# Optimization experiments

Measured on AMD Instinct MI355X. Metric: run time of the kernel, lower is better.

Reference implementation:

```python
import jax, jax.numpy as jnp
import numpy as np

# E2M1 (FP4) value table: low 3 bits magnitude, bit 3 sign (indices 8..15 negative)
FP4_TABLE = jnp.array([0.0, 0.5, 1.0, 1.5, 2.0, 3.0, 4.0, 6.0,
                       0.0, -0.5, -1.0, -1.5, -2.0, -3.0, -4.0, -6.0], dtype=jnp.float32)
FP4_BLOCK = 32  # per-row 1x32 scale groups


def dequant_fp4(packed, scale):
    """packed: [E, O, I//2] uint8 (two e2m1 nibbles per byte, low nibble first),
    scale: [E, O, I//32] float32 (e8m0, i.e. powers of two). Returns [E, O, I] float32."""
    lo = (packed & 15).astype(jnp.int32)
    hi = ((packed >> 4) & 15).astype(jnp.int32)
    # interleave low, high nibbles along the input dim (matches torch stack(...,-1).flatten)
    vals = FP4_TABLE[jnp.stack([lo, hi], axis=-1)]  # [E, O, I//2, 2]
    w = vals.reshape(packed.shape[0], packed.shape[1], packed.shape[2] * 2)
    return w * jnp.repeat(scale, FP4_BLOCK, axis=-1)


def setup_inputs() -> dict:
    T, H, F, E, K = 2048, 2048, 1024, 16, 4
    key = jax.random.key(0)
    k = jax.random.split(key, 8)
    hidden_states = jax.random.normal(k[0], (T, H), dtype=jnp.float32)
    topk_weights = jax.nn.softmax(jax.random.normal(k[1], (T, K)), axis=-1)
    topk_ids = jax.random.randint(k[2], (T, K), 0, E, dtype=jnp.int32)
    # checkpoint-native packed FP4 expert weights + e8m0 (power-of-two) scales
    gate_up_weight = jax.random.randint(k[3], (E, 2 * F, H // 2), 0, 256, dtype=jnp.int32).astype(jnp.uint8)
    gate_up_scale = jnp.exp2(jax.random.randint(k[4], (E, 2 * F, H // 32), -8, -5).astype(jnp.float32))
    down_weight = jax.random.randint(k[5], (E, H, F // 2), 0, 256, dtype=jnp.int32).astype(jnp.uint8)
    down_scale = jnp.exp2(jax.random.randint(k[6], (E, H, F // 32), -8, -5).astype(jnp.float32))
    return {"hidden_states": hidden_states, "topk_weights": topk_weights, "topk_ids": topk_ids,
            "gate_up_weight": gate_up_weight, "gate_up_scale": gate_up_scale,
            "down_weight": down_weight, "down_scale": down_scale}


def reference(hidden_states, topk_weights, topk_ids, gate_up_weight, gate_up_scale, down_weight, down_scale):
    # 1. dequantize checkpoint-native FP4 experts to dense float weights
    w_gate_up = dequant_fp4(gate_up_weight, gate_up_scale)  # [E, 2F, H]
    w_down = dequant_fp4(down_weight, down_scale)           # [E, H, F]
    T = hidden_states.shape[0]
    E = w_gate_up.shape[0]
    # 2. scatter routing weights into a dense [T, E] combine matrix
    combine = jnp.zeros((T, E), dtype=hidden_states.dtype)
    combine = combine.at[jnp.arange(T)[:, None], topk_ids].add(topk_weights)
    # 3. grouped expert GEMM (exact dense dispatch over experts)
    gu = jnp.einsum('th,eoh->teo', hidden_states, w_gate_up)  # [T, E, 2F]
    gate, up = jnp.split(gu, 2, axis=-1)                       # gate = first ffn_dim rows
    act = jax.nn.silu(gate) * up                               # SwiGLU (swiglu_limit=0 -> no clamping)
    act = act * combine[:, :, None]                            # fold routing weights into activations
    return jnp.einsum('tef,ehf->th', act, w_down)              # [T, H]
```

## Files before the change

kernel.cpp:

```cpp
#include <hip/hip_runtime.h>
#include <stdint.h>

#define T_TOK 2048
#define HD 2048
#define FD 1024
#define NE 16
#define NPAIR 8192
#define BM 128
#define MAXTILES 80
#define LDK 40

typedef short bf16x8 __attribute__((ext_vector_type(8)));
typedef float f32x4 __attribute__((ext_vector_type(4)));
typedef unsigned short u16;

static __device__ __forceinline__ u16 f2bf(float f) {
  uint32_t u = __float_as_uint(f);
  u += 0x7FFFu + ((u >> 16) & 1u);
  return (u16)(u >> 16);
}

static __device__ __forceinline__ float fp4_val(uint32_t nib, float scale) {
  uint32_t mag = nib & 7u;
  uint32_t big = ((126u + (mag >> 1)) << 23) | ((mag & 1u) << 22);
  uint32_t small = (0u - (mag & 1u)) & 0x3F000000u;
  uint32_t bits = (mag >= 2u) ? big : small;
  bits |= (nib & 8u) << 28;
  return __uint_as_float(bits) * scale;
}

static __device__ __forceinline__ uint32_t dq_byte(uint32_t b, float scale) {
  float lo = fp4_val(b & 15u, scale);
  float hi = fp4_val((b >> 4) & 15u, scale);
  return ((uint32_t)(__float_as_uint(lo) >> 16)) | (__float_as_uint(hi) & 0xFFFF0000u);
}

__global__ void cast_kernel(const float* __restrict__ x, u16* __restrict__ xb) {
  int i = blockIdx.x * 256 + threadIdx.x;
  float4 v = ((const float4*)x)[i];
  ushort4 o;
  o.x = f2bf(v.x); o.y = f2bf(v.y); o.z = f2bf(v.z); o.w = f2bf(v.w);
  ((ushort4*)xb)[i] = o;
}

__global__ void zero_kernel(float4* __restrict__ out) {
  out[blockIdx.x * 256 + threadIdx.x] = float4{0.f, 0.f, 0.f, 0.f};
}

__global__ void route_kernel(const int* __restrict__ ids, const float* __restrict__ tw,
                             int* __restrict__ rows, float* __restrict__ rw,
                             int* __restrict__ te) {
  __shared__ int cnt[NE], base[NE], run[NE];
  int tid = threadIdx.x;
  if (tid < NE) { cnt[tid] = 0; run[tid] = 0; }
  __syncthreads();
  for (int i = tid; i < NPAIR; i += 256) atomicAdd(&cnt[ids[i]], 1);
  __syncthreads();
  if (tid == 0) {
    int cum = 0;
    for (int e = 0; e < NE; ++e) {
      base[e] = cum;
      int nt = (cnt[e] + BM - 1) >> 7;
      for (int j = 0; j < nt; ++j) te[(cum >> 7) + j] = e;
      cum += nt << 7;
    }
    for (int t = cum >> 7; t < MAXTILES; ++t) te[t] = -1;
  }
  __syncthreads();
  for (int i = tid; i < MAXTILES * BM; i += 256) { rows[i] = -1; rw[i] = 0.f; }
  __syncthreads();
  for (int i = tid; i < NPAIR; i += 256) {
    int e = ids[i];
    int p = base[e] + atomicAdd(&run[e], 1);
    rows[p] = i >> 2;
    rw[p] = tw[i];
  }
}

__global__ __launch_bounds__(256) void gemm1_kernel(
    const u16* __restrict__ xb, const int* __restrict__ gup32,
    const float* __restrict__ gus, const int* __restrict__ rows,
    const float* __restrict__ rw, const int* __restrict__ te,
    u16* __restrict__ act) {
  const int tile = blockIdx.y;
  const int e = te[tile];
  if (e < 0) return;
  const int f0 = blockIdx.x * 64;

  __shared__ u16 sA[BM * LDK];
  __shared__ u16 sBg[64 * LDK];
  __shared__ u16 sBu[64 * LDK];
  __shared__ int rows_s[BM];
  __shared__ float rw_s[BM];

  const int tid = threadIdx.x;
  if (tid < BM) {
    rows_s[tid] = rows[tile * BM + tid];
    rw_s[tid] = rw[tile * BM + tid];
  }
  __syncthreads();

  const int sm = tid >> 1;
  const int skh = tid & 1;
  int arow = rows_s[sm];
  arow = arow < 0 ? 0 : arow;
  const u16* aptr = xb + (size_t)arow * HD + skh * 16;
  u16* sAp = &sA[sm * LDK + skh * 16];

  const int bn = (tid & 127) >> 1;
  const int isUp = tid >> 7;
  const int o = isUp * 1024 + f0 + bn;
  const int* bptr = gup32 + (size_t)(e * 2048 + o) * (HD / 2) + skh * 8;
  const float* sptr = gus + (size_t)(e * 2048 + o) * (HD / 32);
  u16* sBp = (isUp ? sBu : sBg) + bn * LDK + skh * 16;

  const int lane = tid & 63;
  const int wid = tid >> 6;
  const int wm = wid >> 1, wn = wid & 1;
  const int q = lane >> 4, c = lane & 15;

  f32x4 Cg[4][2], Cu[4][2];
#pragma unroll
  for (int s = 0; s < 4; ++s)
#pragma unroll
    for (int t2 = 0; t2 < 2; ++t2) {
      Cg[s][t2] = f32x4{0.f, 0.f, 0.f, 0.f};
      Cu[s][t2] = f32x4{0.f, 0.f, 0.f, 0.f};
    }

  for (int kk = 0; kk < HD; kk += 32) {
    uint4 av0 = *(const uint4*)(aptr + kk);
    uint4 av1 = *(const uint4*)(aptr + kk + 8);
    int4 w0 = *(const int4*)(bptr + (kk >> 1));
    int4 w1 = *(const int4*)(bptr + (kk >> 1) + 4);
    float sc = sptr[kk >> 5];
    uint32_t d[8];
    d[0] = dq_byte((uint32_t)w0.x, sc);
    d[1] = dq_byte((uint32_t)w0.y, sc);
    d[2] = dq_byte((uint32_t)w0.z, sc);
    d[3] = dq_byte((uint32_t)w0.w, sc);
    d[4] = dq_byte((uint32_t)w1.x, sc);
    d[5] = dq_byte((uint32_t)w1.y, sc);
    d[6] = dq_byte((uint32_t)w1.z, sc);
    d[7] = dq_byte((uint32_t)w1.w, sc);
    *(uint4*)sAp = av0;
    *(uint4*)(sAp + 8) = av1;
    *(uint4*)sBp = make_uint4(d[0], d[1], d[2], d[3]);
    *(uint4*)(sBp + 8) = make_uint4(d[4], d[5], d[6], d[7]);
    __syncthreads();

    bf16x8 af[4], bgf[2], buf_[2];
#pragma unroll
    for (int s = 0; s < 4; ++s)
      af[s] = *(const bf16x8*)&sA[(wm * 64 + s * 16 + c) * LDK + q * 8];
#pragma unroll
    for (int t2 = 0; t2 < 2; ++t2) {
      bgf[t2] = *(const bf16x8*)&sBg[(wn * 32 + t2 * 16 + c) * LDK + q * 8];
      buf_[t2] = *(const bf16x8*)&sBu[(wn * 32 + t2 * 16 + c) * LDK + q * 8];
    }
#pragma unroll
    for (int s = 0; s < 4; ++s)
#pragma unroll
      for (int t2 = 0; t2 < 2; ++t2) {
        Cg[s][t2] = __builtin_amdgcn_mfma_f32_16x16x32_bf16(af[s], bgf[t2], Cg[s][t2], 0, 0, 0);
        Cu[s][t2] = __builtin_amdgcn_mfma_f32_16x16x32_bf16(af[s], buf_[t2], Cu[s][t2], 0, 0, 0);
      }
    __syncthreads();
  }

#pragma unroll
  for (int s = 0; s < 4; ++s) {
    const int mlb = wm * 64 + s * 16 + q * 4;
#pragma unroll
    for (int t2 = 0; t2 < 2; ++t2) {
      const int fg = f0 + wn * 32 + t2 * 16 + c;
#pragma unroll
      for (int r = 0; r < 4; ++r) {
        const int ml = mlb + r;
        float g = Cg[s][t2][r];
        float u = Cu[s][t2][r];
        float aval = g / (1.f + __expf(-g)) * u * rw_s[ml];
        act[(size_t)(tile * BM + ml) * FD + fg] = f2bf(aval);
      }
    }
  }
}

__global__ __launch_bounds__(256) void gemm2_kernel(
    const u16* __restrict__ act, const int* __restrict__ dwn32,
    const float* __restrict__ dsc, const int* __restrict__ rows,
    const int* __restrict__ te, float* __restrict__ out) {
  const int tile = blockIdx.y;
  const int e = te[tile];
  if (e < 0) return;
  const int h0 = blockIdx.x * 64;

  __shared__ u16 sA[BM * LDK];
  __shared__ u16 sB[64 * LDK];
  __shared__ int rows_s[BM];

  const int tid = threadIdx.x;
  if (tid < BM) rows_s[tid] = rows[tile * BM + tid];
  __syncthreads();

  const int sm = tid >> 1;
  const int skh = tid & 1;
  const u16* aptr = act + (size_t)(tile * BM + sm) * FD + skh * 16;
  u16* sAp = &sA[sm * LDK + skh * 16];

  const int bn2 = tid >> 2;
  const int kq = tid & 3;
  const int* bptr = dwn32 + (size_t)(e * 2048 + h0 + bn2) * (FD / 2) + kq * 4;
  const float* sptr = dsc + (size_t)(e * 2048 + h0 + bn2) * (FD / 32);
  u16* sBp = &sB[bn2 * LDK + kq * 8];

  const int lane = tid & 63;
  const int wid = tid >> 6;
  const int wm = wid >> 1, wn = wid & 1;
  const int q = lane >> 4, c = lane & 15;

  f32x4 Cd[4][2];
#pragma unroll
  for (int s = 0; s < 4; ++s)
#pragma unroll
    for (int t2 = 0; t2 < 2; ++t2) Cd[s][t2] = f32x4{0.f, 0.f, 0.f, 0.f};

  for (int kk = 0; kk < FD; kk += 32) {
    uint4 av0 = *(const uint4*)(aptr + kk);
    uint4 av1 = *(const uint4*)(aptr + kk + 8);
    int4 w = *(const int4*)(bptr + (kk >> 1));
    float sc = sptr[kk >> 5];
    uint32_t d[4];
    d[0] = dq_byte((uint32_t)w.x, sc);
    d[1] = dq_byte((uint32_t)w.y, sc);
    d[2] = dq_byte((uint32_t)w.z, sc);
    d[3] = dq_byte((uint32_t)w.w, sc);
    *(uint4*)sAp = av0;
    *(uint4*)(sAp + 8) = av1;
    *(uint4*)sBp = make_uint4(d[0], d[1], d[2], d[3]);
    __syncthreads();

    bf16x8 af[4], bf_[2];
#pragma unroll
    for (int s = 0; s < 4; ++s)
      af[s] = *(const bf16x8*)&sA[(wm * 64 + s * 16 + c) * LDK + q * 8];
#pragma unroll
    for (int t2 = 0; t2 < 2; ++t2)
      bf_[t2] = *(const bf16x8*)&sB[(wn * 32 + t2 * 16 + c) * LDK + q * 8];
#pragma unroll
    for (int s = 0; s < 4; ++s)
#pragma unroll
      for (int t2 = 0; t2 < 2; ++t2)
        Cd[s][t2] = __builtin_amdgcn_mfma_f32_16x16x32_bf16(af[s], bf_[t2], Cd[s][t2], 0, 0, 0);
    __syncthreads();
  }

#pragma unroll
  for (int s = 0; s < 4; ++s) {
    const int mlb = wm * 64 + s * 16 + q * 4;
#pragma unroll
    for (int t2 = 0; t2 < 2; ++t2) {
      const int hg = h0 + wn * 32 + t2 * 16 + c;
#pragma unroll
      for (int r = 0; r < 4; ++r) {
        int token = rows_s[mlb + r];
        if (token >= 0) atomicAdd(&out[(size_t)token * HD + hg], Cd[s][t2][r]);
      }
    }
  }
}

extern "C" void kernel_launch(void* const* d_in, const int* in_sizes, int n_in,
                              void* d_out, int out_size, void* d_ws, size_t ws_size,
                              hipStream_t stream) {
  const float* hidden = (const float*)d_in[0];
  const float* tw = (const float*)d_in[1];
  const int* ids = (const int*)d_in[2];
  const int* gup32 = (const int*)d_in[3];
  const float* gus = (const float*)d_in[4];
  const int* dwn32 = (const int*)d_in[5];
  const float* dsc = (const float*)d_in[6];
  float* out = (float*)d_out;

  char* ws = (char*)d_ws;
  int* rows = (int*)(ws);
  float* rw = (float*)(ws + 49152);
  int* te = (int*)(ws + 98304);
  u16* xb = (u16*)(ws + 131072);
  u16* act = (u16*)(ws + 131072 + 8388608);

  cast_kernel<<<dim3(4096), dim3(256), 0, stream>>>(hidden, xb);
  zero_kernel<<<dim3(4096), dim3(256), 0, stream>>>((float4*)out);
  route_kernel<<<dim3(1), dim3(256), 0, stream>>>(ids, tw, rows, rw, te);
  gemm1_kernel<<<dim3(16, MAXTILES), dim3(256), 0, stream>>>(xb, gup32, gus, rows, rw, te, act);
  gemm2_kernel<<<dim3(32, MAXTILES), dim3(256), 0, stream>>>(act, dwn32, dsc, rows, te, out);
}
```

Measured before the change: 597.9 us.

## Enlarge MoE GEMM tiles to 256 rows and dequantize FP4 via byte-permute tables

Raises the routed-token tile from 128 to 256 rows and widens the gemm2 output tile to 128 columns, so each workgroup reuses every dequantized weight tile across more tokens and issues more MFMAs per LDS load. The per-nibble float arithmetic for FP4 dequantization is replaced by a lookup built from v_perm byte tables derived from the e8m0 scale exponent. Launch bounds now request two workgroups per CU. Larger tiles mean more padding rows per expert and more accumulator registers, and the lookup depends on the scales being exact powers of two.

```diff
diff --git a/kernel.cpp b/kernel.cpp
--- a/kernel.cpp
+++ b/kernel.cpp
@@ -1,13 +1,12 @@
 #include <hip/hip_runtime.h>
 #include <stdint.h>
 
-#define T_TOK 2048
 #define HD 2048
 #define FD 1024
 #define NE 16
 #define NPAIR 8192
-#define BM 128
-#define MAXTILES 80
+#define BM 256
+#define MAXT 48
 #define LDK 40
 
 typedef short bf16x8 __attribute__((ext_vector_type(8)));
@@ -20,19 +19,43 @@
   return (u16)(u >> 16);
 }
 
-static __device__ __forceinline__ float fp4_val(uint32_t nib, float scale) {
-  uint32_t mag = nib & 7u;
-  uint32_t big = ((126u + (mag >> 1)) << 23) | ((mag & 1u) << 22);
-  uint32_t small = (0u - (mag & 1u)) & 0x3F000000u;
-  uint32_t bits = (mag >= 2u) ? big : small;
-  bits |= (nib & 8u) << 28;
-  return __uint_as_float(bits) * scale;
-}
-
-static __device__ __forceinline__ uint32_t dq_byte(uint32_t b, float scale) {
-  float lo = fp4_val(b & 15u, scale);
-  float hi = fp4_val((b >> 4) & 15u, scale);
-  return ((uint32_t)(__float_as_uint(lo) >> 16)) | (__float_as_uint(hi) & 0xFFFF0000u);
+struct DqTab { uint32_t hA, hB, lA, lB; };
+
+static __device__ __forceinline__ DqTab make_tab(uint32_t sbits) {
+  int n = (int)(sbits >> 23) - 127;
+  int q = n >> 1;
+  uint32_t r = (uint32_t)(n & 1);
+  uint32_t mq = (uint32_t)(-q);
+  uint32_t sub1 = mq * 0x01010100u;
+  uint32_t subA = mq * 0x01010101u;
+  DqTab t;
+  t.hA = (r ? 0x40403F00u : 0x3F3F3F00u) - sub1;
+  t.hB = (r ? 0x41414040u : 0x40404040u) - subA;
+  t.lA = r ? 0x40008000u : 0xC0800000u;
+  t.lB = r ? 0x4000C080u : 0xC0804000u;
+  return t;
+}
+
+static __device__ __forceinline__ void dq8(uint32_t p, const DqTab& t, uint32_t* d) {
+  uint32_t a = p & 0x0F0F0F0Fu;
+  uint32_t b = (p >> 4) & 0x0F0F0F0Fu;
+  uint32_t x0 = __builtin_amdgcn_perm(b, a, 0x05010400u);
+  uint32_t x1 = __builtin_amdgcn_perm(b, a, 0x07030602u);
+  uint32_t m0 = x0 & 0x07070707u;
+  uint32_t m1 = x1 & 0x07070707u;
+  uint32_t h0 = __builtin_amdgcn_perm(t.hB, t.hA, m0) | ((x0 & 0x08080808u) << 4);
+  uint32_t h1 = __builtin_amdgcn_perm(t.hB, t.hA, m1) | ((x1 & 0x08080808u) << 4);
+  uint32_t l0 = __builtin_amdgcn_perm(t.lB, t.lA, m0);
+  uint32_t l1 = __builtin_amdgcn_perm(t.lB, t.lA, m1);
+  d[0] = __builtin_amdgcn_perm(h0, l0, 0x05010400u);
+  d[1] = __builtin_amdgcn_perm(h0, l0, 0x07030602u);
+  d[2] = __builtin_amdgcn_perm(h1, l1, 0x05010400u);
+  d[3] = __builtin_amdgcn_perm(h1, l1, 0x07030602u);
+}
+
+static __device__ __forceinline__ uint32_t pack4(int4 v) {
+  return (uint32_t)(v.x & 0xFF) | ((uint32_t)(v.y & 0xFF) << 8) |
+         ((uint32_t)(v.z & 0xFF) << 16) | ((uint32_t)v.w << 24);
 }
 
 __global__ void cast_kernel(const float* __restrict__ x, u16* __restrict__ xb) {
@@ -60,14 +83,14 @@
     int cum = 0;
     for (int e = 0; e < NE; ++e) {
       base[e] = cum;
-      int nt = (cnt[e] + BM - 1) >> 7;
-      for (int j = 0; j < nt; ++j) te[(cum >> 7) + j] = e;
-      cum += nt << 7;
-    }
-    for (int t = cum >> 7; t < MAXTILES; ++t) te[t] = -1;
-  }
-  __syncthreads();
-  for (int i = tid; i < MAXTILES * BM; i += 256) { rows[i] = -1; rw[i] = 0.f; }
+      int nt = (cnt[e] + BM - 1) >> 8;
+      for (int j = 0; j < nt; ++j) te[(cum >> 8) + j] = e;
+      cum += nt << 8;
+    }
+    for (int t = cum >> 8; t < MAXT; ++t) te[t] = -1;
+  }
+  __syncthreads();
+  for (int i = tid; i < MAXT * BM; i += 256) { rows[i] = -1; rw[i] = 0.f; }
   __syncthreads();
   for (int i = tid; i < NPAIR; i += 256) {
     int e = ids[i];
@@ -77,9 +100,9 @@
   }
 }
 
-__global__ __launch_bounds__(256) void gemm1_kernel(
+__global__ __launch_bounds__(256, 2) void gemm1_kernel(
     const u16* __restrict__ xb, const int* __restrict__ gup32,
-    const float* __restrict__ gus, const int* __restrict__ rows,
+    const uint32_t* __restrict__ gus, const int* __restrict__ rows,
     const float* __restrict__ rw, const int* __restrict__ te,
     u16* __restrict__ act) {
   const int tile = blockIdx.y;
@@ -94,86 +117,81 @@
   __shared__ float rw_s[BM];
 
   const int tid = threadIdx.x;
-  if (tid < BM) {
-    rows_s[tid] = rows[tile * BM + tid];
-    rw_s[tid] = rw[tile * BM + tid];
-  }
-  __syncthreads();
-
-  const int sm = tid >> 1;
-  const int skh = tid & 1;
-  int arow = rows_s[sm];
+  rows_s[tid] = rows[tile * BM + tid];
+  rw_s[tid] = rw[tile * BM + tid];
+  __syncthreads();
+
+  int arow = rows_s[tid];
   arow = arow < 0 ? 0 : arow;
-  const u16* aptr = xb + (size_t)arow * HD + skh * 16;
-  u16* sAp = &sA[sm * LDK + skh * 16];
+  const u16* aptr = xb + (size_t)arow * HD;
+  u16* sAp = &sA[tid * LDK];
 
   const int bn = (tid & 127) >> 1;
   const int isUp = tid >> 7;
   const int o = isUp * 1024 + f0 + bn;
+  const int skh = tid & 1;
   const int* bptr = gup32 + (size_t)(e * 2048 + o) * (HD / 2) + skh * 8;
-  const float* sptr = gus + (size_t)(e * 2048 + o) * (HD / 32);
+  const uint32_t* sptr = gus + (size_t)(e * 2048 + o) * (HD / 32);
   u16* sBp = (isUp ? sBu : sBg) + bn * LDK + skh * 16;
 
   const int lane = tid & 63;
-  const int wid = tid >> 6;
-  const int wm = wid >> 1, wn = wid & 1;
+  const int w = tid >> 6;
   const int q = lane >> 4, c = lane & 15;
 
-  f32x4 Cg[4][2], Cu[4][2];
+  f32x4 Cg[4][4], Cu[4][4];
 #pragma unroll
   for (int s = 0; s < 4; ++s)
 #pragma unroll
-    for (int t2 = 0; t2 < 2; ++t2) {
+    for (int t2 = 0; t2 < 4; ++t2) {
       Cg[s][t2] = f32x4{0.f, 0.f, 0.f, 0.f};
       Cu[s][t2] = f32x4{0.f, 0.f, 0.f, 0.f};
     }
 
   for (int kk = 0; kk < HD; kk += 32) {
-    uint4 av0 = *(const uint4*)(aptr + kk);
-    uint4 av1 = *(const uint4*)(aptr + kk + 8);
+    uint4 a0 = *(const uint4*)(aptr + kk);
+    uint4 a1 = *(const uint4*)(aptr + kk + 8);
+    uint4 a2 = *(const uint4*)(aptr + kk + 16);
+    uint4 a3 = *(const uint4*)(aptr + kk + 24);
     int4 w0 = *(const int4*)(bptr + (kk >> 1));
     int4 w1 = *(const int4*)(bptr + (kk >> 1) + 4);
-    float sc = sptr[kk >> 5];
-    uint32_t d[8];
-    d[0] = dq_byte((uint32_t)w0.x, sc);
-    d[1] = dq_byte((uint32_t)w0.y, sc);
-    d[2] = dq_byte((uint32_t)w0.z, sc);
-    d[3] = dq_byte((uint32_t)w0.w, sc);
-    d[4] = dq_byte((uint32_t)w1.x, sc);
-    d[5] = dq_byte((uint32_t)w1.y, sc);
-    d[6] = dq_byte((uint32_t)w1.z, sc);
-    d[7] = dq_byte((uint32_t)w1.w, sc);
-    *(uint4*)sAp = av0;
-    *(uint4*)(sAp + 8) = av1;
-    *(uint4*)sBp = make_uint4(d[0], d[1], d[2], d[3]);
-    *(uint4*)(sBp + 8) = make_uint4(d[4], d[5], d[6], d[7]);
+    uint32_t sb = sptr[kk >> 5];
+    DqTab t = make_tab(sb);
+    uint32_t d0[4], d1[4];
+    dq8(pack4(w0), t, d0);
+    dq8(pack4(w1), t, d1);
+    *(uint4*)sAp = a0;
+    *(uint4*)(sAp + 8) = a1;
+    *(uint4*)(sAp + 16) = a2;
+    *(uint4*)(sAp + 24) = a3;
+    *(uint4*)sBp = make_uint4(d0[0], d0[1], d0[2], d0[3]);
+    *(uint4*)(sBp + 8) = make_uint4(d1[0], d1[1], d1[2], d1[3]);
     __syncthreads();
 
-    bf16x8 af[4], bgf[2], buf_[2];
+    bf16x8 af[4], bg[4], bu[4];
 #pragma unroll
     for (int s = 0; s < 4; ++s)
-      af[s] = *(const bf16x8*)&sA[(wm * 64 + s * 16 + c) * LDK + q * 8];
-#pragma unroll
-    for (int t2 = 0; t2 < 2; ++t2) {
-      bgf[t2] = *(const bf16x8*)&sBg[(wn * 32 + t2 * 16 + c) * LDK + q * 8];
-      buf_[t2] = *(const bf16x8*)&sBu[(wn * 32 + t2 * 16 + c) * LDK + q * 8];
+      af[s] = *(const bf16x8*)&sA[(w * 64 + s * 16 + c) * LDK + q * 8];
+#pragma unroll
+    for (int t2 = 0; t2 < 4; ++t2) {
+      bg[t2] = *(const bf16x8*)&sBg[(t2 * 16 + c) * LDK + q * 8];
+      bu[t2] = *(const bf16x8*)&sBu[(t2 * 16 + c) * LDK + q * 8];
     }
 #pragma unroll
     for (int s = 0; s < 4; ++s)
 #pragma unroll
-      for (int t2 = 0; t2 < 2; ++t2) {
-        Cg[s][t2] = __builtin_amdgcn_mfma_f32_16x16x32_bf16(af[s], bgf[t2], Cg[s][t2], 0, 0, 0);
-        Cu[s][t2] = __builtin_amdgcn_mfma_f32_16x16x32_bf16(af[s], buf_[t2], Cu[s][t2], 0, 0, 0);
+      for (int t2 = 0; t2 < 4; ++t2) {
+        Cg[s][t2] = __builtin_amdgcn_mfma_f32_16x16x32_bf16(af[s], bg[t2], Cg[s][t2], 0, 0, 0);
+        Cu[s][t2] = __builtin_amdgcn_mfma_f32_16x16x32_bf16(af[s], bu[t2], Cu[s][t2], 0, 0, 0);
       }
     __syncthreads();
   }
 
 #pragma unroll
   for (int s = 0; s < 4; ++s) {
-    const int mlb = wm * 64 + s * 16 + q * 4;
-#pragma unroll
-    for (int t2 = 0; t2 < 2; ++t2) {
-      const int fg = f0 + wn * 32 + t2 * 16 + c;
+    const int mlb = w * 64 + s * 16 + q * 4;
+#pragma unroll
+    for (int t2 = 0; t2 < 4; ++t2) {
+      const int fg = f0 + t2 * 16 + c;
 #pragma unroll
       for (int r = 0; r < 4; ++r) {
         const int ml = mlb + r;
@@ -186,81 +204,83 @@
   }
 }
 
-__global__ __launch_bounds__(256) void gemm2_kernel(
+__global__ __launch_bounds__(256, 2) void gemm2_kernel(
     const u16* __restrict__ act, const int* __restrict__ dwn32,
-    const float* __restrict__ dsc, const int* __restrict__ rows,
+    const uint32_t* __restrict__ dsc, const int* __restrict__ rows,
     const int* __restrict__ te, float* __restrict__ out) {
   const int tile = blockIdx.y;
   const int e = te[tile];
   if (e < 0) return;
-  const int h0 = blockIdx.x * 64;
+  const int h0 = blockIdx.x * 128;
 
   __shared__ u16 sA[BM * LDK];
-  __shared__ u16 sB[64 * LDK];
+  __shared__ u16 sB[128 * LDK];
   __shared__ int rows_s[BM];
 
   const int tid = threadIdx.x;
-  if (tid < BM) rows_s[tid] = rows[tile * BM + tid];
-  __syncthreads();
-
-  const int sm = tid >> 1;
+  rows_s[tid] = rows[tile * BM + tid];
+  __syncthreads();
+
+  const u16* aptr = act + (size_t)(tile * BM + tid) * FD;
+  u16* sAp = &sA[tid * LDK];
+
+  const int bn = tid >> 1;
   const int skh = tid & 1;
-  const u16* aptr = act + (size_t)(tile * BM + sm) * FD + skh * 16;
-  u16* sAp = &sA[sm * LDK + skh * 16];
-
-  const int bn2 = tid >> 2;
-  const int kq = tid & 3;
-  const int* bptr = dwn32 + (size_t)(e * 2048 + h0 + bn2) * (FD / 2) + kq * 4;
-  const float* sptr = dsc + (size_t)(e * 2048 + h0 + bn2) * (FD / 32);
-  u16* sBp = &sB[bn2 * LDK + kq * 8];
+  const int* bptr = dwn32 + (size_t)(e * 2048 + h0 + bn) * (FD / 2) + skh * 8;
+  const uint32_t* sptr = dsc + (size_t)(e * 2048 + h0 + bn) * (FD / 32);
+  u16* sBp = &sB[bn * LDK + skh * 16];
 
   const int lane = tid & 63;
-  const int wid = tid >> 6;
-  const int wm = wid >> 1, wn = wid & 1;
+  const int w = tid >> 6;
   const int q = lane >> 4, c = lane & 15;
 
-  f32x4 Cd[4][2];
+  f32x4 Cd[4][8];
 #pragma unroll
   for (int s = 0; s < 4; ++s)
 #pragma unroll
-    for (int t2 = 0; t2 < 2; ++t2) Cd[s][t2] = f32x4{0.f, 0.f, 0.f, 0.f};
+    for (int t2 = 0; t2 < 8; ++t2) Cd[s][t2] = f32x4{0.f, 0.f, 0.f, 0.f};
 
   for (int kk = 0; kk < FD; kk += 32) {
-    uint4 av0 = *(const uint4*)(aptr + kk);
-    uint4 av1 = *(const uint4*)(aptr + kk + 8);
-    int4 w = *(const int4*)(bptr + (kk >> 1));
-    float sc = sptr[kk >> 5];
-    uint32_t d[4];
-    d[0] = dq_byte((uint32_t)w.x, sc);
-    d[1] = dq_byte((uint32_t)w.y, sc);
-    d[2] = dq_byte((uint32_t)w.z, sc);
-    d[3] = dq_byte((uint32_t)w.w, sc);
-    *(uint4*)sAp = av0;
-    *(uint4*)(sAp + 8) = av1;
-    *(uint4*)sBp = make_uint4(d[0], d[1], d[2], d[3]);
+    uint4 a0 = *(const uint4*)(aptr + kk);
+    uint4 a1 = *(const uint4*)(aptr + kk + 8);
+    uint4 a2 = *(const uint4*)(aptr + kk + 16);
+    uint4 a3 = *(const uint4*)(aptr + kk + 24);
+    int4 w0 = *(const int4*)(bptr + (kk >> 1));
+    int4 w1 = *(const int4*)(bptr + (kk >> 1) + 4);
+    uint32_t sb = sptr[kk >> 5];
+    DqTab t = make_tab(sb);
+    uint32_t d0[4], d1[4];
+    dq8(pack4(w0), t, d0);
+    dq8(pack4(w1), t, d1);
+    *(uint4*)sAp = a0;
+    *(uint4*)(sAp + 8) = a1;
+    *(uint4*)(sAp + 16) = a2;
+    *(uint4*)(sAp + 24) = a3;
+    *(uint4*)sBp = make_uint4(d0[0], d0[1], d0[2], d0[3]);
+    *(uint4*)(sBp + 8) = make_uint4(d1[0], d1[1], d1[2], d1[3]);
     __syncthreads();
 
-    bf16x8 af[4], bf_[2];
+    bf16x8 af[4], bf_[8];
 #pragma unroll
     for (int s = 0; s < 4; ++s)
-      af[s] = *(const bf16x8*)&sA[(wm * 64 + s * 16 + c) * LDK + q * 8];
-#pragma unroll
-    for (int t2 = 0; t2 < 2; ++t2)
-      bf_[t2] = *(const bf16x8*)&sB[(wn * 32 + t2 * 16 + c) * LDK + q * 8];
+      af[s] = *(const bf16x8*)&sA[(w * 64 + s * 16 + c) * LDK + q * 8];
+#pragma unroll
+    for (int t2 = 0; t2 < 8; ++t2)
+      bf_[t2] = *(const bf16x8*)&sB[(t2 * 16 + c) * LDK + q * 8];
 #pragma unroll
     for (int s = 0; s < 4; ++s)
 #pragma unroll
-      for (int t2 = 0; t2 < 2; ++t2)
+      for (int t2 = 0; t2 < 8; ++t2)
         Cd[s][t2] = __builtin_amdgcn_mfma_f32_16x16x32_bf16(af[s], bf_[t2], Cd[s][t2], 0, 0, 0);
     __syncthreads();
   }
 
 #pragma unroll
   for (int s = 0; s < 4; ++s) {
-    const int mlb = wm * 64 + s * 16 + q * 4;
-#pragma unroll
-    for (int t2 = 0; t2 < 2; ++t2) {
-      const int hg = h0 + wn * 32 + t2 * 16 + c;
+    const int mlb = w * 64 + s * 16 + q * 4;
+#pragma unroll
+    for (int t2 = 0; t2 < 8; ++t2) {
+      const int hg = h0 + t2 * 16 + c;
 #pragma unroll
       for (int r = 0; r < 4; ++r) {
         int token = rows_s[mlb + r];
@@ -277,9 +297,9 @@
   const float* tw = (const float*)d_in[1];
   const int* ids = (const int*)d_in[2];
   const int* gup32 = (const int*)d_in[3];
-  const float* gus = (const float*)d_in[4];
+  const uint32_t* gus = (const uint32_t*)d_in[4];
   const int* dwn32 = (const int*)d_in[5];
-  const float* dsc = (const float*)d_in[6];
+  const uint32_t* dsc = (const uint32_t*)d_in[6];
   float* out = (float*)d_out;
 
   char* ws = (char*)d_ws;
@@ -287,11 +307,11 @@
   float* rw = (float*)(ws + 49152);
   int* te = (int*)(ws + 98304);
   u16* xb = (u16*)(ws + 131072);
-  u16* act = (u16*)(ws + 131072 + 8388608);
+  u16* act = (u16*)(ws + 8519680);
 
   cast_kernel<<<dim3(4096), dim3(256), 0, stream>>>(hidden, xb);
   zero_kernel<<<dim3(4096), dim3(256), 0, stream>>>((float4*)out);
   route_kernel<<<dim3(1), dim3(256), 0, stream>>>(ids, tw, rows, rw, te);
-  gemm1_kernel<<<dim3(16, MAXTILES), dim3(256), 0, stream>>>(xb, gup32, gus, rows, rw, te, act);
-  gemm2_kernel<<<dim3(32, MAXTILES), dim3(256), 0, stream>>>(act, dwn32, dsc, rows, te, out);
-}
+  gemm1_kernel<<<dim3(16, MAXT), dim3(256), 0, stream>>>(xb, gup32, gus, rows, rw, te, act);
+  gemm2_kernel<<<dim3(16, MAXT), dim3(256), 0, stream>>>(act, dwn32, dsc, rows, te, out);
+}
```

Result: slower. 613.7 us (+2.6%).
